# Kernel optimization log

Hardware: AMD Instinct MI355X
Metric: run time of the kernel (lower is better)

## Reference

```python
import jax, jax.numpy as jnp
import numpy as np

B, T, C = 2, 2048, 1024
E, H, TOPK = 8, 2048, 2


def setup_inputs() -> dict:
    key = jax.random.key(0)
    k0, k1, k2, k3 = jax.random.split(key, 4)
    scale = 0.02
    return {
        "x": jax.random.normal(k0, (B, T, C), dtype=jnp.float32),
        "Wg": jax.random.normal(k1, (C, E), dtype=jnp.float32) * scale,
        "W1": jax.random.normal(k2, (E, C, H), dtype=jnp.float32) * scale,
        "W2": jax.random.normal(k3, (E, H, C), dtype=jnp.float32) * scale,
    }


def reference(x, Wg, W1, W2):
    b, t, c = x.shape
    xf = x.reshape(-1, c)                      # [N, C]
    n = xf.shape[0]
    scores = xf @ Wg                            # [N, E]
    topk_scores, topk_idx = jax.lax.top_k(scores, TOPK)   # [N, K]
    topk_probs = jax.nn.softmax(topk_scores, axis=-1)     # [N, K]
    # scatter top-k probs into dense combine weights [N, E] (same math as the
    # per-expert masked gather/scatter loop in the original)
    combine = jnp.zeros((n, E), dtype=xf.dtype)
    combine = combine.at[jnp.arange(n)[:, None], topk_idx].set(topk_probs)
    # run every expert on all tokens, then weight-combine (zero weight for
    # non-selected experts reproduces the routed computation exactly)
    h = jnp.einsum("nc,ech->enh", xf, W1)       # [E, N, H]
    h = jax.nn.silu(h)
    eo = jnp.einsum("enh,ehc->enc", h, W2)      # [E, N, C]
    y = jnp.einsum("ne,enc->nc", combine, eo)   # [N, C]
    return y.reshape(b, t, c)
```

## Files before the change

### kernel.cpp

```cpp
#include <hip/hip_runtime.h>
#include <hip/hip_bf16.h>

#define NB 2
#define NT 2048
#define NC 1024
#define NE 8
#define NH 2048
#define NN (NB*NT)
#define NSLOT (NN*2)

typedef short s16x8 __attribute__((ext_vector_type(8)));
typedef float f32x4 __attribute__((ext_vector_type(4)));

__device__ __forceinline__ unsigned short f2bf(float f) {
  union { float f; unsigned int u; } v; v.f = f;
  unsigned int r = v.u + 0x7FFFu + ((v.u >> 16) & 1u);
  return (unsigned short)(r >> 16);
}

#define GLOAD_LDS16(gp, lp) \
  __builtin_amdgcn_global_load_lds( \
      (const __attribute__((address_space(1))) void*)(gp), \
      (__attribute__((address_space(3))) void*)(lp), 16, 0, 0)

__global__ void cvt_kernel(const float* __restrict__ in,
                           unsigned short* __restrict__ out, int n4) {
  int i = blockIdx.x * blockDim.x + threadIdx.x;
  if (i >= n4) return;
  float4 v = ((const float4*)in)[i];
  ushort4 o;
  o.x = f2bf(v.x); o.y = f2bf(v.y); o.z = f2bf(v.z); o.w = f2bf(v.w);
  ((ushort4*)out)[i] = o;
}

__global__ void tcvt_kernel(const float* __restrict__ in,
                            unsigned short* __restrict__ out, int R, int Cc) {
  __shared__ unsigned short tile[32][33];
  const size_t eb = (size_t)blockIdx.z * R * Cc;
  const float* ip = in + eb;
  unsigned short* op = out + eb;
  const int c0 = blockIdx.x * 32, r0 = blockIdx.y * 32;
  const int t = threadIdx.x;
  {
    const int r = t >> 3, c4 = (t & 7) * 4;
    float4 v = *(const float4*)(ip + (size_t)(r0 + r) * Cc + c0 + c4);
    tile[r][c4 + 0] = f2bf(v.x); tile[r][c4 + 1] = f2bf(v.y);
    tile[r][c4 + 2] = f2bf(v.z); tile[r][c4 + 3] = f2bf(v.w);
  }
  __syncthreads();
  {
    const int c = t >> 3, q = (t & 7) * 4;
    ushort4 o;
    o.x = tile[q + 0][c]; o.y = tile[q + 1][c];
    o.z = tile[q + 2][c]; o.w = tile[q + 3][c];
    *(ushort4*)(op + (size_t)(c0 + c) * R + r0 + q) = o;
  }
}

__global__ void router_kernel(const float* __restrict__ x, const float* __restrict__ Wg,
                              int* __restrict__ tk_idx, float* __restrict__ tk_p) {
  int lane = threadIdx.x & 63;
  int n = blockIdx.x * 4 + (threadIdx.x >> 6);
  const float4* xr = (const float4*)(x + (size_t)n * NC);
  float sc[NE];
  #pragma unroll
  for (int e = 0; e < NE; ++e) sc[e] = 0.f;
  #pragma unroll
  for (int i = 0; i < NC / 4 / 64; ++i) {
    int c4 = i * 64 + lane;
    float4 xv = xr[c4];
    const float4* wr = (const float4*)(Wg + (size_t)c4 * 4 * NE);
    #pragma unroll
    for (int j = 0; j < 4; ++j) {
      float xj = (j == 0) ? xv.x : (j == 1) ? xv.y : (j == 2) ? xv.z : xv.w;
      float4 w0 = wr[j * 2], w1 = wr[j * 2 + 1];
      sc[0] += xj * w0.x; sc[1] += xj * w0.y; sc[2] += xj * w0.z; sc[3] += xj * w0.w;
      sc[4] += xj * w1.x; sc[5] += xj * w1.y; sc[6] += xj * w1.z; sc[7] += xj * w1.w;
    }
  }
  #pragma unroll
  for (int e = 0; e < NE; ++e) {
    float v = sc[e];
    for (int s = 32; s >= 1; s >>= 1) v += __shfl_xor(v, s);
    sc[e] = v;
  }
  if (lane == 0) {
    int i0 = 0;
    #pragma unroll
    for (int e = 1; e < NE; ++e) if (sc[e] > sc[i0]) i0 = e;
    int i1 = (i0 == 0) ? 1 : 0;
    #pragma unroll
    for (int e = 0; e < NE; ++e) if (e != i0 && sc[e] > sc[i1]) i1 = e;
    float e1 = __expf(sc[i1] - sc[i0]);
    float inv = 1.f / (1.f + e1);
    tk_idx[n * 2] = i0; tk_idx[n * 2 + 1] = i1;
    tk_p[n * 2] = inv;  tk_p[n * 2 + 1] = e1 * inv;
  }
}

__global__ void route_scan_scatter(const int* __restrict__ tk_idx,
                                   const float* __restrict__ tk_p,
                                   int* __restrict__ offs,
                                   int* __restrict__ slot_token,
                                   float* __restrict__ slot_w,
                                   int* __restrict__ slot_of) {
  __shared__ int wcnt[4][NE];
  __shared__ int basel[4][NE];
  const int lane = threadIdx.x & 63, w = threadIdx.x >> 6;
  const unsigned long long lt = (1ull << lane) - 1ull;

  int cnt0 = 0, cnt1 = 0, cnt2 = 0, cnt3 = 0, cnt4 = 0, cnt5 = 0, cnt6 = 0, cnt7 = 0;
  for (int ch = 0; ch < 32; ++ch) {
    int entry = (w * 32 + ch) * 64 + lane;
    int em = tk_idx[entry];
    cnt0 += __popcll(__ballot(em == 0));
    cnt1 += __popcll(__ballot(em == 1));
    cnt2 += __popcll(__ballot(em == 2));
    cnt3 += __popcll(__ballot(em == 3));
    cnt4 += __popcll(__ballot(em == 4));
    cnt5 += __popcll(__ballot(em == 5));
    cnt6 += __popcll(__ballot(em == 6));
    cnt7 += __popcll(__ballot(em == 7));
  }
  if (lane < NE) {
    int v = 0;
    if (lane == 0) v = cnt0; if (lane == 1) v = cnt1;
    if (lane == 2) v = cnt2; if (lane == 3) v = cnt3;
    if (lane == 4) v = cnt4; if (lane == 5) v = cnt5;
    if (lane == 6) v = cnt6; if (lane == 7) v = cnt7;
    wcnt[w][lane] = v;
  }
  __syncthreads();

  if (threadIdx.x == 0) {
    int a = 0;
    for (int e = 0; e < NE; ++e) {
      offs[e] = a;
      int s = a;
      for (int w2 = 0; w2 < 4; ++w2) { basel[w2][e] = s; s += wcnt[w2][e]; }
      a = s;
    }
    offs[NE] = a;
  }
  __syncthreads();

  int rb0 = basel[w][0], rb1 = basel[w][1], rb2 = basel[w][2], rb3 = basel[w][3];
  int rb4 = basel[w][4], rb5 = basel[w][5], rb6 = basel[w][6], rb7 = basel[w][7];
  for (int ch = 0; ch < 32; ++ch) {
    int entry = (w * 32 + ch) * 64 + lane;
    int em = tk_idx[entry];
    int pos = 0;
    unsigned long long m;
    m = __ballot(em == 0); if (em == 0) pos = rb0 + __popcll(m & lt); rb0 += __popcll(m);
    m = __ballot(em == 1); if (em == 1) pos = rb1 + __popcll(m & lt); rb1 += __popcll(m);
    m = __ballot(em == 2); if (em == 2) pos = rb2 + __popcll(m & lt); rb2 += __popcll(m);
    m = __ballot(em == 3); if (em == 3) pos = rb3 + __popcll(m & lt); rb3 += __popcll(m);
    m = __ballot(em == 4); if (em == 4) pos = rb4 + __popcll(m & lt); rb4 += __popcll(m);
    m = __ballot(em == 5); if (em == 5) pos = rb5 + __popcll(m & lt); rb5 += __popcll(m);
    m = __ballot(em == 6); if (em == 6) pos = rb6 + __popcll(m & lt); rb6 += __popcll(m);
    m = __ballot(em == 7); if (em == 7) pos = rb7 + __popcll(m & lt); rb7 += __popcll(m);
    slot_token[pos] = entry >> 1;
    slot_w[pos] = tk_p[entry];
    slot_of[entry] = pos;
  }
}

template <int SILU, int GATHER>
__global__ __launch_bounds__(256, 2) void moe_gemm_kernel(
    const unsigned short* __restrict__ A, const unsigned short* __restrict__ Bt,
    void* __restrict__ Out, const int* __restrict__ slot_token,
    const float* __restrict__ slot_w, const int* __restrict__ offs, int K, int Nn) {
  __shared__ unsigned short lds_a[128 * 64];
  __shared__ unsigned short lds_b[128 * 64];

  const int gx = gridDim.x;
  const int h = blockIdx.x + gx * (blockIdx.y + gridDim.y * blockIdx.z);
  const int xcd = h & 7, s = h >> 3;
  const int n_idx = s % gx;
  const int chunk = xcd * ((gridDim.y * gridDim.z) >> 3) + s / gx;
  const int by = chunk & (gridDim.y - 1);
  const int e = chunk >> 5;

  const int off = offs[e];
  const int me = offs[e + 1] - off;
  const int rbase = by * 128;
  if (rbase >= me) return;
  const int n0 = n_idx * 128;
  const int tid = threadIdx.x, lane = tid & 63, w = tid >> 6;
  const int wm = w >> 1, wn = w & 1;

  const int lr = lane >> 3;
  const int lq = lane & 7;
  const int sq = (lq ^ lr) * 16;
  const char* srcA[4];
  const char* srcB[4];
  #pragma unroll
  for (int i = 0; i < 4; ++i) {
    const int gr = rbase + w * 32 + i * 8 + lr;
    int ar;
    if (GATHER) ar = (gr < me) ? slot_token[off + gr] : 0;
    else        ar = (gr < me) ? (off + gr) : 0;
    srcA[i] = (const char*)(A + (size_t)ar * K) + sq;
    const int br = n0 + w * 32 + i * 8 + lr;
    srcB[i] = (const char*)(Bt + ((size_t)e * Nn + br) * K) + sq;
  }
  char* la = (char*)lds_a;
  char* lb = (char*)lds_b;

  f32x4 zero = {0.f, 0.f, 0.f, 0.f};
  f32x4 acc[4][4];
  #pragma unroll
  for (int m = 0; m < 4; ++m)
    #pragma unroll
    for (int n = 0; n < 4; ++n) acc[m][n] = zero;

  const int ra = (wm * 64 + (lane & 15)) * 128;
  const int rb = (wn * 64 + (lane & 15)) * 128;
  const int qs0 = (((lane >> 4) + 0) ^ (lane & 7)) * 16;
  const int qs1 = (((lane >> 4) + 4) ^ (lane & 7)) * 16;

  for (int k0 = 0; k0 < K; k0 += 64) {
    const int kb = k0 * 2;
    #pragma unroll
    for (int i = 0; i < 4; ++i) GLOAD_LDS16(srcA[i] + kb, la + w * 4096 + i * 1024);
    #pragma unroll
    for (int i = 0; i < 4; ++i) GLOAD_LDS16(srcB[i] + kb, lb + w * 4096 + i * 1024);
    __syncthreads();
    #pragma unroll
    for (int ks = 0; ks < 2; ++ks) {
      const int qo = ks ? qs1 : qs0;
      s16x8 a[4], b[4];
      #pragma unroll
      for (int m = 0; m < 4; ++m) a[m] = *(const s16x8*)(la + ra + m * 2048 + qo);
      #pragma unroll
      for (int n = 0; n < 4; ++n) b[n] = *(const s16x8*)(lb + rb + n * 2048 + qo);
      #pragma unroll
      for (int m = 0; m < 4; ++m)
        #pragma unroll
        for (int n = 0; n < 4; ++n)
          acc[m][n] = __builtin_amdgcn_mfma_f32_16x16x32_bf16(a[m], b[n], acc[m][n], 0, 0, 0);
    }
    __syncthreads();
  }

  if (SILU) {
    unsigned short* O = (unsigned short*)Out;
    #pragma unroll
    for (int m = 0; m < 4; ++m)
      #pragma unroll
      for (int r = 0; r < 4; ++r) {
        int row = wm * 64 + m * 16 + ((lane >> 4) << 2) + r;
        if (rbase + row < me) {
          size_t base = (size_t)(off + rbase + row) * Nn + n0 + wn * 64 + (lane & 15);
          #pragma unroll
          for (int n = 0; n < 4; ++n) {
            float v = acc[m][n][r];
            O[base + n * 16] = f2bf(v / (1.f + __expf(-v)));
          }
        }
      }
  } else {
    float* O = (float*)Out;
    #pragma unroll
    for (int m = 0; m < 4; ++m)
      #pragma unroll
      for (int r = 0; r < 4; ++r) {
        int row = wm * 64 + m * 16 + ((lane >> 4) << 2) + r;
        if (rbase + row < me) {
          float p = slot_w[off + rbase + row];
          size_t base = (size_t)(off + rbase + row) * Nn + n0 + wn * 64 + (lane & 15);
          #pragma unroll
          for (int n = 0; n < 4; ++n) O[base + n * 16] = p * acc[m][n][r];
        }
      }
  }
}

__global__ void combine_kernel(const float* __restrict__ Eo, const int* __restrict__ slot_of,
                               float* __restrict__ y) {
  int n = blockIdx.x;
  int t = threadIdx.x;
  int s0 = slot_of[n * 2], s1 = slot_of[n * 2 + 1];
  float4 va = ((const float4*)(Eo + (size_t)s0 * NC))[t];
  float4 vb = ((const float4*)(Eo + (size_t)s1 * NC))[t];
  float4 o;
  o.x = va.x + vb.x; o.y = va.y + vb.y; o.z = va.z + vb.z; o.w = va.w + vb.w;
  ((float4*)(y + (size_t)n * NC))[t] = o;
}

extern "C" void kernel_launch(void* const* d_in, const int* in_sizes, int n_in,
                              void* d_out, int out_size, void* d_ws, size_t ws_size,
                              hipStream_t stream) {
  const float* x  = (const float*)d_in[0];
  const float* Wg = (const float*)d_in[1];
  const float* W1 = (const float*)d_in[2];
  const float* W2 = (const float*)d_in[3];
  float* y = (float*)d_out;

  char* p = (char*)d_ws;
  auto carve = [&](size_t bytes) {
    char* r = p;
    p += (bytes + 255) & ~(size_t)255;
    return r;
  };
  unsigned short* xbf  = (unsigned short*)carve((size_t)NN * NC * 2);
  unsigned short* w1t  = (unsigned short*)carve((size_t)NE * NH * NC * 2);
  unsigned short* w2t  = (unsigned short*)carve((size_t)NE * NC * NH * 2);
  unsigned short* hbuf = (unsigned short*)carve((size_t)NSLOT * NH * 2);
  float* eo = (float*)w1t;
  int*   tk_idx     = (int*)carve(NSLOT * 4);
  float* tk_p       = (float*)carve(NSLOT * 4);
  int*   slot_token = (int*)carve(NSLOT * 4);
  float* slot_w     = (float*)carve(NSLOT * 4);
  int*   slot_of    = (int*)carve(NSLOT * 4);
  int*   offs       = (int*)carve((NE + 1) * 4);

  cvt_kernel<<<dim3(NN * NC / 4 / 256), 256, 0, stream>>>(x, xbf, NN * NC / 4);
  tcvt_kernel<<<dim3(NH / 32, NC / 32, NE), 256, 0, stream>>>(W1, w1t, NC, NH);
  tcvt_kernel<<<dim3(NC / 32, NH / 32, NE), 256, 0, stream>>>(W2, w2t, NH, NC);

  router_kernel<<<dim3(NN / 4), 256, 0, stream>>>(x, Wg, tk_idx, tk_p);
  route_scan_scatter<<<1, 256, 0, stream>>>(tk_idx, tk_p, offs,
                                            slot_token, slot_w, slot_of);

  moe_gemm_kernel<1, 1><<<dim3(NH / 128, NN / 128, NE), 256, 0, stream>>>(
      xbf, w1t, hbuf, slot_token, slot_w, offs, NC, NH);
  moe_gemm_kernel<0, 0><<<dim3(NC / 128, NN / 128, NE), 256, 0, stream>>>(
      hbuf, w2t, eo, slot_token, slot_w, offs, NH, NC);

  combine_kernel<<<dim3(NN), 256, 0, stream>>>(eo, slot_of, y);
}
```

Measured before the change: 324.7 us.

## Fuse x conversion into router, widen transpose tiles, raise scan and GEMM occupancy

Drops the standalone fp32-to-bf16 conversion of x and does it inside the router kernel, which already reads x, saving one kernel launch and one full read of x. The weight transpose-convert kernel moves to 64x64 tiles with 16-byte vector stores. The routing scan now runs with 1024 threads instead of 256, and the expert GEMM launch bound asks for 4 blocks per SM instead of 2, which may push the compiler to limit registers and cause spills.

```diff
diff --git a/kernel.cpp b/kernel.cpp
--- a/kernel.cpp
+++ b/kernel.cpp
@@ -10,6 +10,7 @@
 #define NSLOT (NN*2)
 
 typedef short s16x8 __attribute__((ext_vector_type(8)));
+typedef unsigned short u16x8 __attribute__((ext_vector_type(8)));
 typedef float f32x4 __attribute__((ext_vector_type(4)));
 
 __device__ __forceinline__ unsigned short f2bf(float f) {
@@ -23,45 +24,39 @@
       (const __attribute__((address_space(1))) void*)(gp), \
       (__attribute__((address_space(3))) void*)(lp), 16, 0, 0)
 
-__global__ void cvt_kernel(const float* __restrict__ in,
-                           unsigned short* __restrict__ out, int n4) {
-  int i = blockIdx.x * blockDim.x + threadIdx.x;
-  if (i >= n4) return;
-  float4 v = ((const float4*)in)[i];
-  ushort4 o;
-  o.x = f2bf(v.x); o.y = f2bf(v.y); o.z = f2bf(v.z); o.w = f2bf(v.w);
-  ((ushort4*)out)[i] = o;
-}
-
-__global__ void tcvt_kernel(const float* __restrict__ in,
-                            unsigned short* __restrict__ out, int R, int Cc) {
-  __shared__ unsigned short tile[32][33];
+__global__ void tcvt64_kernel(const float* __restrict__ in,
+                              unsigned short* __restrict__ out, int R, int Cc) {
+  __shared__ unsigned short tileT[64][72];
   const size_t eb = (size_t)blockIdx.z * R * Cc;
   const float* ip = in + eb;
   unsigned short* op = out + eb;
-  const int c0 = blockIdx.x * 32, r0 = blockIdx.y * 32;
+  const int c0 = blockIdx.x * 64, r0 = blockIdx.y * 64;
   const int t = threadIdx.x;
-  {
-    const int r = t >> 3, c4 = (t & 7) * 4;
+  #pragma unroll
+  for (int i = 0; i < 4; ++i) {
+    const int slot = i * 256 + t;
+    const int r = slot >> 4, c4 = (slot & 15) * 4;
     float4 v = *(const float4*)(ip + (size_t)(r0 + r) * Cc + c0 + c4);
-    tile[r][c4 + 0] = f2bf(v.x); tile[r][c4 + 1] = f2bf(v.y);
-    tile[r][c4 + 2] = f2bf(v.z); tile[r][c4 + 3] = f2bf(v.w);
+    tileT[c4 + 0][r] = f2bf(v.x); tileT[c4 + 1][r] = f2bf(v.y);
+    tileT[c4 + 2][r] = f2bf(v.z); tileT[c4 + 3][r] = f2bf(v.w);
   }
   __syncthreads();
-  {
-    const int c = t >> 3, q = (t & 7) * 4;
-    ushort4 o;
-    o.x = tile[q + 0][c]; o.y = tile[q + 1][c];
-    o.z = tile[q + 2][c]; o.w = tile[q + 3][c];
-    *(ushort4*)(op + (size_t)(c0 + c) * R + r0 + q) = o;
+  #pragma unroll
+  for (int i = 0; i < 2; ++i) {
+    const int slot = i * 256 + t;
+    const int c = slot >> 3, r8 = (slot & 7) * 8;
+    u16x8 v = *(const u16x8*)&tileT[c][r8];
+    *(u16x8*)(op + (size_t)(c0 + c) * R + r0 + r8) = v;
   }
 }
 
 __global__ void router_kernel(const float* __restrict__ x, const float* __restrict__ Wg,
+                              unsigned short* __restrict__ xbf,
                               int* __restrict__ tk_idx, float* __restrict__ tk_p) {
   int lane = threadIdx.x & 63;
   int n = blockIdx.x * 4 + (threadIdx.x >> 6);
   const float4* xr = (const float4*)(x + (size_t)n * NC);
+  unsigned short* xo = xbf + (size_t)n * NC;
   float sc[NE];
   #pragma unroll
   for (int e = 0; e < NE; ++e) sc[e] = 0.f;
@@ -69,6 +64,9 @@
   for (int i = 0; i < NC / 4 / 64; ++i) {
     int c4 = i * 64 + lane;
     float4 xv = xr[c4];
+    ushort4 o;
+    o.x = f2bf(xv.x); o.y = f2bf(xv.y); o.z = f2bf(xv.z); o.w = f2bf(xv.w);
+    *(ushort4*)(xo + c4 * 4) = o;
     const float4* wr = (const float4*)(Wg + (size_t)c4 * 4 * NE);
     #pragma unroll
     for (int j = 0; j < 4; ++j) {
@@ -104,14 +102,14 @@
                                    int* __restrict__ slot_token,
                                    float* __restrict__ slot_w,
                                    int* __restrict__ slot_of) {
-  __shared__ int wcnt[4][NE];
-  __shared__ int basel[4][NE];
+  __shared__ int wcnt[16][NE];
+  __shared__ int basel[16][NE];
   const int lane = threadIdx.x & 63, w = threadIdx.x >> 6;
   const unsigned long long lt = (1ull << lane) - 1ull;
 
   int cnt0 = 0, cnt1 = 0, cnt2 = 0, cnt3 = 0, cnt4 = 0, cnt5 = 0, cnt6 = 0, cnt7 = 0;
-  for (int ch = 0; ch < 32; ++ch) {
-    int entry = (w * 32 + ch) * 64 + lane;
+  for (int ch = 0; ch < 8; ++ch) {
+    int entry = (w * 8 + ch) * 64 + lane;
     int em = tk_idx[entry];
     cnt0 += __popcll(__ballot(em == 0));
     cnt1 += __popcll(__ballot(em == 1));
@@ -137,7 +135,7 @@
     for (int e = 0; e < NE; ++e) {
       offs[e] = a;
       int s = a;
-      for (int w2 = 0; w2 < 4; ++w2) { basel[w2][e] = s; s += wcnt[w2][e]; }
+      for (int w2 = 0; w2 < 16; ++w2) { basel[w2][e] = s; s += wcnt[w2][e]; }
       a = s;
     }
     offs[NE] = a;
@@ -146,8 +144,8 @@
 
   int rb0 = basel[w][0], rb1 = basel[w][1], rb2 = basel[w][2], rb3 = basel[w][3];
   int rb4 = basel[w][4], rb5 = basel[w][5], rb6 = basel[w][6], rb7 = basel[w][7];
-  for (int ch = 0; ch < 32; ++ch) {
-    int entry = (w * 32 + ch) * 64 + lane;
+  for (int ch = 0; ch < 8; ++ch) {
+    int entry = (w * 8 + ch) * 64 + lane;
     int em = tk_idx[entry];
     int pos = 0;
     unsigned long long m;
@@ -166,7 +164,7 @@
 }
 
 template <int SILU, int GATHER>
-__global__ __launch_bounds__(256, 2) void moe_gemm_kernel(
+__global__ __launch_bounds__(256, 4) void moe_gemm_kernel(
     const unsigned short* __restrict__ A, const unsigned short* __restrict__ Bt,
     void* __restrict__ Out, const int* __restrict__ slot_token,
     const float* __restrict__ slot_w, const int* __restrict__ offs, int K, int Nn) {
@@ -315,13 +313,12 @@
   int*   slot_of    = (int*)carve(NSLOT * 4);
   int*   offs       = (int*)carve((NE + 1) * 4);
 
-  cvt_kernel<<<dim3(NN * NC / 4 / 256), 256, 0, stream>>>(x, xbf, NN * NC / 4);
-  tcvt_kernel<<<dim3(NH / 32, NC / 32, NE), 256, 0, stream>>>(W1, w1t, NC, NH);
-  tcvt_kernel<<<dim3(NC / 32, NH / 32, NE), 256, 0, stream>>>(W2, w2t, NH, NC);
-
-  router_kernel<<<dim3(NN / 4), 256, 0, stream>>>(x, Wg, tk_idx, tk_p);
-  route_scan_scatter<<<1, 256, 0, stream>>>(tk_idx, tk_p, offs,
-                                            slot_token, slot_w, slot_of);
+  tcvt64_kernel<<<dim3(NH / 64, NC / 64, NE), 256, 0, stream>>>(W1, w1t, NC, NH);
+  tcvt64_kernel<<<dim3(NC / 64, NH / 64, NE), 256, 0, stream>>>(W2, w2t, NH, NC);
+
+  router_kernel<<<dim3(NN / 4), 256, 0, stream>>>(x, Wg, xbf, tk_idx, tk_p);
+  route_scan_scatter<<<1, 1024, 0, stream>>>(tk_idx, tk_p, offs,
+                                             slot_token, slot_w, slot_of);
 
   moe_gemm_kernel<1, 1><<<dim3(NH / 128, NN / 128, NE), 256, 0, stream>>>(
       xbf, w1t, hbuf, slot_token, slot_w, offs, NC, NH);
```

Result: faster. 300.0 us (-7.6%).
